# Kernel tuning notes

Hardware: AMD Instinct MI355X
Metric: run time of the kernel (lower is better)

Reference implementation:

```python
import jax, jax.numpy as jnp
import numpy as np

B, S, D_IN, E, H = 2, 2048, 1024, 1024, 16  # batch, seq, input_size, embedding_size, heads


def setup_inputs() -> dict:
    key = jax.random.key(0)
    k1, k2, k3 = jax.random.split(key, 3)
    x = jax.random.normal(k1, (B, S, D_IN), dtype=jnp.float32)
    # fused QKV projection weight stored as [in, 3E] (torch Linear weight transposed)
    W0 = jax.random.normal(k2, (D_IN, 3 * E), dtype=jnp.float32) * (1.0 / np.sqrt(D_IN))
    b0 = jax.random.normal(k3, (3 * E,), dtype=jnp.float32) * 0.02
    return {"x": x, "W0": W0, "b0": b0}


def reference(x, W0, b0):
    b, s, _ = x.shape
    y = x @ W0 + b0                              # [B,S,3E]
    y = y.reshape(b, s, H, -1).transpose(0, 2, 1, 3)  # [B,H,S,3*head_dim]
    q, k, v = jnp.split(y, 3, axis=-1)           # each [B,H,S,head_dim]
    scale = 1.0 / jnp.sqrt(jnp.asarray(D_IN, dtype=x.dtype))  # NB: sqrt(input_size), as in source
    scores = jnp.einsum("bhqd,bhkd->bhqk", q, k) * scale
    # causal mask: -inf above diagonal
    causal = jnp.triu(jnp.full((s, s), -jnp.inf, dtype=scores.dtype), k=1)
    scores = scores + causal
    attn = jax.nn.softmax(scores, axis=-1)       # [B,H,S,S]
    o = jnp.einsum("bhqk,bhkd->bhqd", attn, v)   # [B,H,S,head_dim]
    # faithful to source: reshape directly from (B,H,S,d) to (B,S,H*d) WITHOUT permuting back
    return o.reshape(b, s, -1)
```

## Files before the change

kernel.cpp:

```cpp
#include <hip/hip_runtime.h>
#include <stdint.h>

typedef __attribute__((ext_vector_type(4))) float f32x4;
typedef __attribute__((ext_vector_type(16))) float f32x16;
typedef __attribute__((ext_vector_type(8))) short bf16x8;
typedef __attribute__((ext_vector_type(4))) short bf16x4;

#define MFMA16(a, b, c) __builtin_amdgcn_mfma_f32_16x16x32_bf16((a), (b), (c), 0, 0, 0)
#define MFMA32(a, b, c) __builtin_amdgcn_mfma_f32_32x32x16_bf16((a), (b), (c), 0, 0, 0)

__device__ __forceinline__ short f2bf(float f) {
    union { float f; uint32_t u; } v; v.f = f;
    uint32_t r = (v.u + 0x7fffu + ((v.u >> 16) & 1u)) >> 16;
    return (short)(uint16_t)r;
}
__device__ __forceinline__ float bf2f(short s) {
    union { uint32_t u; float f; } v; v.u = ((uint32_t)(uint16_t)s) << 16;
    return v.f;
}
__device__ __forceinline__ float fast_exp2(float x) {
    float r; asm("v_exp_f32 %0, %1" : "=v"(r) : "v"(x)); return r;
}

__device__ __forceinline__ void async_ld16(const short* g, short* l) {
    __builtin_amdgcn_global_load_lds(
        (const __attribute__((address_space(1))) uint32_t*)g,
        (__attribute__((address_space(3))) uint32_t*)l, 16, 0, 0);
}

#define MK_BFRAG(C, O, OUT) do {                                                   \
    uint32_t a_, b_, c_, d_;                                                       \
    asm("v_cvt_pk_bf16_f32 %0, %1, %2" : "=v"(a_) : "v"((C)[(O)+0]), "v"((C)[(O)+1])); \
    asm("v_cvt_pk_bf16_f32 %0, %1, %2" : "=v"(c_) : "v"((C)[(O)+2]), "v"((C)[(O)+3])); \
    asm("v_cvt_pk_bf16_f32 %0, %1, %2" : "=v"(b_) : "v"((C)[(O)+4]), "v"((C)[(O)+5])); \
    asm("v_cvt_pk_bf16_f32 %0, %1, %2" : "=v"(d_) : "v"((C)[(O)+6]), "v"((C)[(O)+7])); \
    asm("v_permlane32_swap_b32 %0, %1" : "+v"(a_), "+v"(b_));                      \
    asm("v_permlane32_swap_b32 %0, %1" : "+v"(c_), "+v"(d_));                      \
    union { uint32_t u[4]; bf16x8 v; } pb_;                                        \
    pb_.u[0] = a_; pb_.u[1] = c_; pb_.u[2] = b_; pb_.u[3] = d_;                    \
    OUT = pb_.v;                                                                   \
} while (0)

__global__ __launch_bounds__(256)
void convert_x(const float* __restrict__ X, short* __restrict__ Xb) {
    const int i8 = (blockIdx.x * 256 + threadIdx.x) << 3;
    f32x4 a = *(const f32x4*)(X + i8);
    f32x4 b = *(const f32x4*)(X + i8 + 4);
    bf16x8 o;
#pragma unroll
    for (int j = 0; j < 4; ++j) { o[j] = f2bf(a[j]); o[4 + j] = f2bf(b[j]); }
    *(bf16x8*)(Xb + i8) = o;
}

__global__ __launch_bounds__(256)
void convert_wt(const float* __restrict__ W, short* __restrict__ Wt) {
    __shared__ short T[64][72];
    const int t = threadIdx.x;
    const int n0 = blockIdx.x * 64, k0 = blockIdx.y * 64;
#pragma unroll
    for (int i = 0; i < 4; ++i) {
        const int r = i * 16 + (t >> 4);
        const int c = (t & 15) << 2;
        f32x4 v = *(const f32x4*)(W + (size_t)(k0 + r) * 3072 + n0 + c);
#pragma unroll
        for (int j = 0; j < 4; ++j) T[c + j][r] = f2bf(v[j]);
    }
    __syncthreads();
#pragma unroll
    for (int i = 0; i < 2; ++i) {
        const int r = i * 32 + (t >> 3);
        const int c = (t & 7) << 3;
        *(bf16x8*)(Wt + (size_t)(n0 + r) * 1024 + k0 + c) = *(const bf16x8*)&T[r][c];
    }
}

__global__ __launch_bounds__(256, 3)
void gemm_pack(const short* __restrict__ Xb, const short* __restrict__ Wt,
               const float* __restrict__ bias, short* __restrict__ Qp,
               short* __restrict__ Kp, short* __restrict__ Vp) {
    __shared__ short Asm[3][128 * 32];
    __shared__ short Bsm[3][128 * 32];

    const int tid  = threadIdx.x;
    const int lane = tid & 63;
    const int l15  = lane & 15;
    const int lq   = lane >> 4;
    const int wave = tid >> 6;
    const int wr = wave >> 1, wc = wave & 1;

    const int bid = blockIdx.x;
    const int swz = (bid & 7) * 96 + (bid >> 3);
    const int m0 = (swz / 24) * 128, n0 = (swz % 24) * 128;

    const int srow = tid >> 2;
    const int scolsw = (((tid & 3) ^ (srow & 3)) << 3);

    f32x4 acc[4][4];
#pragma unroll
    for (int m = 0; m < 4; ++m)
#pragma unroll
        for (int n = 0; n < 4; ++n) acc[m][n] = (f32x4)(0.0f);

    auto stage = [&](int k0, int bb) {
#pragma unroll
        for (int i = 0; i < 2; ++i)
            async_ld16(Xb + (size_t)(m0 + i * 64 + srow) * 1024 + k0 + scolsw,
                       &Asm[bb][(i * 256 + wave * 64) * 8]);
#pragma unroll
        for (int i = 0; i < 2; ++i)
            async_ld16(Wt + (size_t)(n0 + i * 64 + srow) * 1024 + k0 + scolsw,
                       &Bsm[bb][(i * 256 + wave * 64) * 8]);
    };

    const int gsw = ((lq ^ (l15 & 3)) << 3);

    auto compute = [&](int bb) {
        bf16x8 af[4], bfv[4];
#pragma unroll
        for (int m = 0; m < 4; ++m)
            af[m] = *(const bf16x8*)&Asm[bb][(wr * 64 + m * 16 + l15) * 32 + gsw];
#pragma unroll
        for (int n = 0; n < 4; ++n)
            bfv[n] = *(const bf16x8*)&Bsm[bb][(wc * 64 + n * 16 + l15) * 32 + gsw];
#pragma unroll
        for (int m = 0; m < 4; ++m)
#pragma unroll
            for (int n = 0; n < 4; ++n) acc[m][n] = MFMA16(af[m], bfv[n], acc[m][n]);
    };

#define WAITV(N) do {                                           \
        asm volatile("s_waitcnt vmcnt(" #N ")" ::: "memory");   \
        __builtin_amdgcn_sched_barrier(0);                      \
        __builtin_amdgcn_s_barrier();                           \
        __builtin_amdgcn_sched_barrier(0);                      \
    } while (0)

    stage(0, 0);
    stage(32, 1);
#pragma unroll 1
    for (int kt = 0; kt < 30; ++kt) {
        WAITV(4);
        compute(kt % 3);
        stage((kt + 2) * 32, (kt + 2) % 3);
    }
    WAITV(4);
    compute(0);
    WAITV(0);
    compute(1);
#undef WAITV

    const float SCALE2 = 0.03125f * 1.44269504f;
    float bv[4];
#pragma unroll
    for (int n = 0; n < 4; ++n) bv[n] = bias[n0 + wc * 64 + n * 16 + l15];

    const size_t bbase = (size_t)(m0 >> 11) * 2097152;
    const int tokb = (m0 & 2047) + wr * 64;

#pragma unroll
    for (int n = 0; n < 4; ++n) {
        const int col = n0 + wc * 64 + n * 16 + l15;
        const int h   = col / 192;
        const int seg = (col >> 6) % 3;
        const int d   = col & 63;
        const size_t hb = bbase + (size_t)h * 131072;
        if (seg == 0) {
            const int cp = ((d >> 4) << 9) + (((d >> 3) & 1) << 8) + (d & 7);
#pragma unroll
            for (int m = 0; m < 4; ++m)
#pragma unroll
                for (int r = 0; r < 4; ++r) {
                    const int tok = tokb + m * 16 + (lq << 2) + r;
                    Qp[hb + ((size_t)(tok >> 5) << 11) + ((tok & 31) << 3) + cp] =
                        f2bf((acc[m][n][r] + bv[n]) * SCALE2);
                }
        } else if (seg == 1) {
            const int cp = ((d >> 4) << 10) + (((d >> 3) & 1) << 8) + (d & 7);
#pragma unroll
            for (int m = 0; m < 4; ++m)
#pragma unroll
                for (int r = 0; r < 4; ++r) {
                    const int tok = tokb + m * 16 + (lq << 2) + r;
                    Kp[hb + ((size_t)(tok >> 6) << 12) + (((tok >> 5) & 1) << 9)
                       + ((tok & 31) << 3) + cp] = f2bf(acc[m][n][r] + bv[n]);
                }
        } else {
            const int cp = ((d >> 5) << 11) + ((d & 31) << 3);
#pragma unroll
            for (int m = 0; m < 4; ++m)
#pragma unroll
                for (int r = 0; r < 4; ++r) {
                    const int tok = tokb + m * 16 + (lq << 2) + r;
                    Vp[hb + ((size_t)(tok >> 6) << 12) + (((tok >> 4) & 3) << 9)
                       + (((tok >> 3) & 1) << 8) + (tok & 7) + cp] =
                        f2bf(acc[m][n][r] + bv[n]);
                }
        }
    }
}

__global__ __launch_bounds__(64, 2)
void attn_part(const short* __restrict__ Qp, const short* __restrict__ Kp,
               const short* __restrict__ Vp, short* __restrict__ Po,
               float* __restrict__ Pm) {
    const int tid = threadIdx.x;
    const int l31 = tid & 31;
    const int hi  = tid >> 5;

    const int id  = blockIdx.x;
    const int xcd = id & 7;
    const int idx = id >> 3;
    const int bh  = xcd * 4 + idx / 96;
    const int u   = idx % 96;

    int qt, t0, t1;
    if (u < 32)      { qt = u + 32; t0 = 0;  t1 = 16; }
    else if (u < 64) { qt = 95 - u; t0 = 16; t1 = (qt >> 1) + 1; }
    else             { qt = u - 64; t0 = 0;  t1 = (qt >> 1) + 1; }
    const bool hasDiag = (u >= 32);
    const int q0 = qt * 32;

    const size_t hb = (size_t)bh * 131072;

    bf16x8 qf[4];
    {
        const short* qp = Qp + hb + qt * 2048 + tid * 8;
#pragma unroll
        for (int dg = 0; dg < 4; ++dg) qf[dg] = *(const bf16x8*)(qp + dg * 512);
    }

    f32x16 o0 = (f32x16)(0.f), o1 = (f32x16)(0.f);
    float m_run = -1e30f, l_run = 0.f;
    const int qg = q0 + l31;

    bf16x8 kA[8], kB[8], va[8];

    auto loadK = [&](bf16x8 (&kr)[8], int t) {
        const short* p = Kp + hb + (size_t)t * 4096 + tid * 8;
#pragma unroll
        for (int f = 0; f < 8; ++f)
            kr[f] = *(const bf16x8*)(p + (f >> 1) * 1024 + (f & 1) * 512);
    };
    auto loadV = [&](int t) {
        const short* p = Vp + hb + (size_t)t * 4096 + tid * 8;
#pragma unroll
        for (int f = 0; f < 8; ++f) va[f] = *(const bf16x8*)(p + f * 512);
    };
    auto qk = [&](bf16x8 (&kr)[8], f32x16& c0, f32x16& c1) {
#pragma unroll
        for (int dg = 0; dg < 4; ++dg) {
            c0 = MFMA32(kr[2 * dg],     qf[dg], c0);
            c1 = MFMA32(kr[2 * dg + 1], qf[dg], c1);
        }
    };

    auto smpv = [&](f32x16& c0, f32x16& c1, int kv0, bool DIAG) {
        if (DIAG) {
#pragma unroll
            for (int r = 0; r < 16; ++r) {
                const int kvr = kv0 + (r & 3) + 8 * (r >> 2) + 4 * hi;
                if (kvr > qg)      c0[r] = -1e30f;
                if (kvr + 32 > qg) c1[r] = -1e30f;
            }
        }

        float mr[8];
#pragma unroll
        for (int r = 0; r < 8; ++r)
            mr[r] = fmaxf(fmaxf(c0[r], c0[8 + r]), fmaxf(c1[r], c1[8 + r]));
        float mx = fmaxf(fmaxf(fmaxf(mr[0], mr[1]), fmaxf(mr[2], mr[3])),
                         fmaxf(fmaxf(mr[4], mr[5]), fmaxf(mr[6], mr[7])));
        mx = fmaxf(mx, __shfl_xor(mx, 32, 64));

        if (!__all(mx <= m_run + 8.f)) {
            const float mnew = fmaxf(m_run, mx);
            const float corr = fast_exp2(m_run - mnew);
            l_run *= corr;
            o0 = o0 * corr;
            o1 = o1 * corr;
            m_run = mnew;
        }

        float ps0 = 0.f, ps1 = 0.f, ps2 = 0.f, ps3 = 0.f;
#pragma unroll
        for (int r = 0; r < 4; ++r) {
            c0[r]      = fast_exp2(c0[r]      - m_run); ps0 += c0[r];
            c0[4 + r]  = fast_exp2(c0[4 + r]  - m_run); ps1 += c0[4 + r];
            c0[8 + r]  = fast_exp2(c0[8 + r]  - m_run); ps2 += c0[8 + r];
            c0[12 + r] = fast_exp2(c0[12 + r] - m_run); ps3 += c0[12 + r];
        }
#pragma unroll
        for (int r = 0; r < 4; ++r) {
            c1[r]      = fast_exp2(c1[r]      - m_run); ps0 += c1[r];
            c1[4 + r]  = fast_exp2(c1[4 + r]  - m_run); ps1 += c1[4 + r];
            c1[8 + r]  = fast_exp2(c1[8 + r]  - m_run); ps2 += c1[8 + r];
            c1[12 + r] = fast_exp2(c1[12 + r] - m_run); ps3 += c1[12 + r];
        }
        l_run += (ps0 + ps1) + (ps2 + ps3);

        bf16x8 bf00, bf01, bf10, bf11;
        MK_BFRAG(c0, 0, bf00);
        MK_BFRAG(c0, 8, bf01);
        MK_BFRAG(c1, 0, bf10);
        MK_BFRAG(c1, 8, bf11);

        o0 = MFMA32(va[0], bf00, o0);
        o0 = MFMA32(va[1], bf01, o0);
        o0 = MFMA32(va[2], bf10, o0);
        o0 = MFMA32(va[3], bf11, o0);
        o1 = MFMA32(va[4], bf00, o1);
        o1 = MFMA32(va[5], bf01, o1);
        o1 = MFMA32(va[6], bf10, o1);
        o1 = MFMA32(va[7], bf11, o1);
    };

    int t = t0;
    loadK(kA, t0);
#pragma unroll 1
    for (; t + 2 < t1; t += 2) {
        f32x16 c0 = (f32x16)(0.f), c1 = (f32x16)(0.f);
        qk(kA, c0, c1);
        loadK(kB, t + 1);
        loadV(t);
        smpv(c0, c1, t * 64, false);
        f32x16 d0 = (f32x16)(0.f), d1 = (f32x16)(0.f);
        qk(kB, d0, d1);
        loadK(kA, t + 2);
        loadV(t + 1);
        smpv(d0, d1, (t + 1) * 64, false);
    }
    if (t + 1 < t1) {
        f32x16 c0 = (f32x16)(0.f), c1 = (f32x16)(0.f);
        qk(kA, c0, c1);
        loadK(kB, t + 1);
        loadV(t);
        smpv(c0, c1, t * 64, false);
        f32x16 d0 = (f32x16)(0.f), d1 = (f32x16)(0.f);
        qk(kB, d0, d1);
        loadV(t + 1);
        smpv(d0, d1, (t + 1) * 64, hasDiag);
    } else {
        f32x16 c0 = (f32x16)(0.f), c1 = (f32x16)(0.f);
        qk(kA, c0, c1);
        loadV(t);
        smpv(c0, c1, t * 64, hasDiag);
    }

    const float l_tot = l_run + __shfl_xor(l_run, 32, 64);
    const float inv = 1.f / l_tot;
    const int prow = (bh * 96 + u) * 32 + l31;
#pragma unroll
    for (int g = 0; g < 4; ++g) {
        bf16x4 w4;
#pragma unroll
        for (int j = 0; j < 4; ++j) w4[j] = f2bf(o0[g * 4 + j] * inv);
        *(bf16x4*)&Po[(size_t)prow * 64 + 8 * g + 4 * hi] = w4;
#pragma unroll
        for (int j = 0; j < 4; ++j) w4[j] = f2bf(o1[g * 4 + j] * inv);
        *(bf16x4*)&Po[(size_t)prow * 64 + 32 + 8 * g + 4 * hi] = w4;
    }
    if (hi == 0) Pm[prow] = m_run + __log2f(l_tot);
}

__global__ __launch_bounds__(256)
void attn_combine(const short* __restrict__ Po, const float* __restrict__ Pm,
                  float* __restrict__ Out) {
    const int idx = blockIdx.x * 256 + threadIdx.x;
    const int d4 = (idx & 15) << 2;
    const int rg = idx >> 4;
    const int q  = rg & 2047;
    const int bh = rg >> 11;
    const int qt32 = q >> 5, r = q & 31;

    f32x4 ov;
    if (qt32 < 32) {
        const int p0 = (bh * 96 + 64 + qt32) * 32 + r;
        bf16x4 a = *(const bf16x4*)&Po[(size_t)p0 * 64 + d4];
#pragma unroll
        for (int j = 0; j < 4; ++j) ov[j] = bf2f(a[j]);
    } else {
        const int p0 = (bh * 96 + (qt32 - 32)) * 32 + r;
        const int p1 = (bh * 96 + (95 - qt32)) * 32 + r;
        bf16x4 a = *(const bf16x4*)&Po[(size_t)p0 * 64 + d4];
        bf16x4 c = *(const bf16x4*)&Po[(size_t)p1 * 64 + d4];
        const float m0 = Pm[p0], m1 = Pm[p1];
        const float M = fmaxf(m0, m1);
        const float w0 = exp2f(m0 - M), w1 = exp2f(m1 - M);
        const float inv = 1.f / (w0 + w1);
#pragma unroll
        for (int j = 0; j < 4; ++j) ov[j] = (w0 * bf2f(a[j]) + w1 * bf2f(c[j])) * inv;
    }
    *(f32x4*)&Out[(size_t)rg * 64 + d4] = ov;
}

extern "C" void kernel_launch(void* const* d_in, const int* in_sizes, int n_in,
                              void* d_out, int out_size, void* d_ws, size_t ws_size,
                              hipStream_t stream) {
    const float* x  = (const float*)d_in[0];
    const float* W0 = (const float*)d_in[1];
    const float* b0 = (const float*)d_in[2];
    float* out = (float*)d_out;
    char* ws = (char*)d_ws;

    const size_t SEG_B = (size_t)32 * 131072 * 2;
    const size_t QKV_B = 3 * SEG_B;
    const size_t XBF_B = (size_t)4096 * 1024 * 2;
    const size_t PO_B  = (size_t)32 * 96 * 32 * 64 * 2;

    short* qp = (short*)ws;
    short* kp = (short*)(ws + SEG_B);
    short* vp = (short*)(ws + 2 * SEG_B);
    short* xb = (short*)(ws + QKV_B);
    short* wt = (short*)(ws + QKV_B + XBF_B);
    short* po = (short*)(ws + QKV_B);
    float* pm = (float*)(ws + QKV_B + PO_B);

    convert_x<<<dim3(2048), dim3(256), 0, stream>>>(x, xb);
    convert_wt<<<dim3(48, 16), dim3(256), 0, stream>>>(W0, wt);
    gemm_pack<<<dim3(768), dim3(256), 0, stream>>>(xb, wt, b0, qp, kp, vp);
    attn_part<<<dim3(3072), dim3(64), 0, stream>>>(qp, kp, vp, po, pm);
    attn_combine<<<dim3(4096), dim3(256), 0, stream>>>(po, pm, out);
}
```

Measured before the change: 94.53 us.

## Fuse conversion kernels and pack four heads per attention block

Merges the x and weight bf16 conversion kernels into a single launch, with blocks beyond 2048 handling the weight transpose. It also changes attn_part from 64-thread blocks to 256-thread blocks, where each wave handles a different head for the same query-tile schedule, cutting the grid from 3072 to 768 blocks. The aim is less launch overhead and fewer, larger workgroups. The cost is that the four waves in a block run independent work with no shared data, so a block holds its CU slot until its slowest wave finishes. Occupancy now depends on the (256,2) launch bound rather than the old (64,2).

```diff
diff --git a/kernel.cpp b/kernel.cpp
--- a/kernel.cpp
+++ b/kernel.cpp
@@ -42,21 +42,23 @@
 } while (0)
 
 __global__ __launch_bounds__(256)
-void convert_x(const float* __restrict__ X, short* __restrict__ Xb) {
-    const int i8 = (blockIdx.x * 256 + threadIdx.x) << 3;
-    f32x4 a = *(const f32x4*)(X + i8);
-    f32x4 b = *(const f32x4*)(X + i8 + 4);
-    bf16x8 o;
-#pragma unroll
-    for (int j = 0; j < 4; ++j) { o[j] = f2bf(a[j]); o[4 + j] = f2bf(b[j]); }
-    *(bf16x8*)(Xb + i8) = o;
-}
-
-__global__ __launch_bounds__(256)
-void convert_wt(const float* __restrict__ W, short* __restrict__ Wt) {
+void convert_fused(const float* __restrict__ X, short* __restrict__ Xb,
+                   const float* __restrict__ W, short* __restrict__ Wt) {
     __shared__ short T[64][72];
     const int t = threadIdx.x;
-    const int n0 = blockIdx.x * 64, k0 = blockIdx.y * 64;
+    const int id = blockIdx.x;
+    if (id < 2048) {
+        const int i8 = (id * 256 + t) << 3;
+        f32x4 a = *(const f32x4*)(X + i8);
+        f32x4 b = *(const f32x4*)(X + i8 + 4);
+        bf16x8 o;
+#pragma unroll
+        for (int j = 0; j < 4; ++j) { o[j] = f2bf(a[j]); o[4 + j] = f2bf(b[j]); }
+        *(bf16x8*)(Xb + i8) = o;
+        return;
+    }
+    const int wid = id - 2048;
+    const int n0 = (wid % 48) * 64, k0 = (wid / 48) * 64;
 #pragma unroll
     for (int i = 0; i < 4; ++i) {
         const int r = i * 16 + (t >> 4);
@@ -199,19 +201,20 @@
     }
 }
 
-__global__ __launch_bounds__(64, 2)
+__global__ __launch_bounds__(256, 2)
 void attn_part(const short* __restrict__ Qp, const short* __restrict__ Kp,
                const short* __restrict__ Vp, short* __restrict__ Po,
                float* __restrict__ Pm) {
-    const int tid = threadIdx.x;
-    const int l31 = tid & 31;
-    const int hi  = tid >> 5;
+    const int tid  = threadIdx.x;
+    const int lane = tid & 63;
+    const int l31  = lane & 31;
+    const int hi   = (lane >> 5) & 1;
+    const int w    = tid >> 6;
 
     const int id  = blockIdx.x;
     const int xcd = id & 7;
-    const int idx = id >> 3;
-    const int bh  = xcd * 4 + idx / 96;
-    const int u   = idx % 96;
+    const int u   = id >> 3;
+    const int bh  = xcd * 4 + w;
 
     int qt, t0, t1;
     if (u < 32)      { qt = u + 32; t0 = 0;  t1 = 16; }
@@ -224,7 +227,7 @@
 
     bf16x8 qf[4];
     {
-        const short* qp = Qp + hb + qt * 2048 + tid * 8;
+        const short* qp = Qp + hb + qt * 2048 + lane * 8;
 #pragma unroll
         for (int dg = 0; dg < 4; ++dg) qf[dg] = *(const bf16x8*)(qp + dg * 512);
     }
@@ -236,13 +239,13 @@
     bf16x8 kA[8], kB[8], va[8];
 
     auto loadK = [&](bf16x8 (&kr)[8], int t) {
-        const short* p = Kp + hb + (size_t)t * 4096 + tid * 8;
+        const short* p = Kp + hb + (size_t)t * 4096 + lane * 8;
 #pragma unroll
         for (int f = 0; f < 8; ++f)
             kr[f] = *(const bf16x8*)(p + (f >> 1) * 1024 + (f & 1) * 512);
     };
     auto loadV = [&](int t) {
-        const short* p = Vp + hb + (size_t)t * 4096 + tid * 8;
+        const short* p = Vp + hb + (size_t)t * 4096 + lane * 8;
 #pragma unroll
         for (int f = 0; f < 8; ++f) va[f] = *(const bf16x8*)(p + f * 512);
     };
@@ -415,9 +418,8 @@
     short* po = (short*)(ws + QKV_B);
     float* pm = (float*)(ws + QKV_B + PO_B);
 
-    convert_x<<<dim3(2048), dim3(256), 0, stream>>>(x, xb);
-    convert_wt<<<dim3(48, 16), dim3(256), 0, stream>>>(W0, wt);
+    convert_fused<<<dim3(2816), dim3(256), 0, stream>>>(x, xb, W0, wt);
     gemm_pack<<<dim3(768), dim3(256), 0, stream>>>(xb, wt, b0, qp, kp, vp);
-    attn_part<<<dim3(3072), dim3(64), 0, stream>>>(qp, kp, vp, po, pm);
+    attn_part<<<dim3(768), dim3(256), 0, stream>>>(qp, kp, vp, po, pm);
     attn_combine<<<dim3(4096), dim3(256), 0, stream>>>(po, pm, out);
 }
```

New measurement: 94.04 us. Within noise of the previous version (-0.5%).

## Fuse conversion kernels, reorder attention work items, raise attn occupancy

Applied to the files above, without the earlier changes.

Merges the x and weight conversion kernels into one launch, removing one kernel launch and its tail. Reorders the attention work-item mapping so heads are interleaved within each XCD and diagonal tiles are grouped by cost, with the combine kernel's index math updated to match. Raises attn_part's waves-per-EU hint from 2 to 4, which may force register spills in exchange for more resident waves.

```diff
diff --git a/kernel.cpp b/kernel.cpp
--- a/kernel.cpp
+++ b/kernel.cpp
@@ -42,21 +42,23 @@
 } while (0)
 
 __global__ __launch_bounds__(256)
-void convert_x(const float* __restrict__ X, short* __restrict__ Xb) {
-    const int i8 = (blockIdx.x * 256 + threadIdx.x) << 3;
-    f32x4 a = *(const f32x4*)(X + i8);
-    f32x4 b = *(const f32x4*)(X + i8 + 4);
-    bf16x8 o;
-#pragma unroll
-    for (int j = 0; j < 4; ++j) { o[j] = f2bf(a[j]); o[4 + j] = f2bf(b[j]); }
-    *(bf16x8*)(Xb + i8) = o;
-}
-
-__global__ __launch_bounds__(256)
-void convert_wt(const float* __restrict__ W, short* __restrict__ Wt) {
+void convert_fused(const float* __restrict__ X, short* __restrict__ Xb,
+                   const float* __restrict__ W, short* __restrict__ Wt) {
     __shared__ short T[64][72];
     const int t = threadIdx.x;
-    const int n0 = blockIdx.x * 64, k0 = blockIdx.y * 64;
+    const int id = blockIdx.x;
+    if (id < 2048) {
+        const int i8 = (id * 256 + t) << 3;
+        f32x4 a = *(const f32x4*)(X + i8);
+        f32x4 b = *(const f32x4*)(X + i8 + 4);
+        bf16x8 o;
+#pragma unroll
+        for (int j = 0; j < 4; ++j) { o[j] = f2bf(a[j]); o[4 + j] = f2bf(b[j]); }
+        *(bf16x8*)(Xb + i8) = o;
+        return;
+    }
+    const int wid = id - 2048;
+    const int n0 = (wid % 48) * 64, k0 = (wid / 48) * 64;
 #pragma unroll
     for (int i = 0; i < 4; ++i) {
         const int r = i * 16 + (t >> 4);
@@ -199,7 +201,7 @@
     }
 }
 
-__global__ __launch_bounds__(64, 2)
+__global__ __launch_bounds__(64, 4)
 void attn_part(const short* __restrict__ Qp, const short* __restrict__ Kp,
                const short* __restrict__ Vp, short* __restrict__ Po,
                float* __restrict__ Pm) {
@@ -210,14 +212,20 @@
     const int id  = blockIdx.x;
     const int xcd = id & 7;
     const int idx = id >> 3;
-    const int bh  = xcd * 4 + idx / 96;
-    const int u   = idx % 96;
+    const int u   = idx >> 2;
+    const int bh  = xcd * 4 + (idx & 3);
 
     int qt, t0, t1;
-    if (u < 32)      { qt = u + 32; t0 = 0;  t1 = 16; }
-    else if (u < 64) { qt = 95 - u; t0 = 16; t1 = (qt >> 1) + 1; }
-    else             { qt = u - 64; t0 = 0;  t1 = (qt >> 1) + 1; }
-    const bool hasDiag = (u >= 32);
+    bool hasDiag;
+    if (u < 32) {
+        qt = u + 32; t0 = 0; t1 = 16; hasDiag = false;
+    } else {
+        const int s = 16 - ((u - 32) >> 2);
+        const int j = (u - 32) & 3;
+        if (j < 2) { qt = 2 * s - 2 + j;       t0 = 0;  t1 = s; }
+        else       { qt = 2 * s + 30 + (j - 2); t0 = 16; t1 = s + 16; }
+        hasDiag = true;
+    }
     const int q0 = qt * 32;
 
     const size_t hb = (size_t)bh * 131072;
@@ -357,7 +365,7 @@
         *(bf16x4*)&Po[(size_t)prow * 64 + 8 * g + 4 * hi] = w4;
 #pragma unroll
         for (int j = 0; j < 4; ++j) w4[j] = f2bf(o1[g * 4 + j] * inv);
-        *(bf16x4*)&Po[(size_t)prow * 64 + 32 + 8 * g + 4 * hi] = w4;
+        *(bf16x4*)&Po[(size_t)prow * 64 + 32 + 4 * hi + 8 * g] = w4;
     }
     if (hi == 0) Pm[prow] = m_run + __log2f(l_tot);
 }
@@ -370,17 +378,22 @@
     const int rg = idx >> 4;
     const int q  = rg & 2047;
     const int bh = rg >> 11;
-    const int qt32 = q >> 5, r = q & 31;
+    const int qt = q >> 5, r = q & 31;
 
     f32x4 ov;
-    if (qt32 < 32) {
-        const int p0 = (bh * 96 + 64 + qt32) * 32 + r;
+    if (qt < 32) {
+        const int s = (qt >> 1) + 1;
+        const int u = 32 + (16 - s) * 4 + (qt & 1);
+        const int p0 = (bh * 96 + u) * 32 + r;
         bf16x4 a = *(const bf16x4*)&Po[(size_t)p0 * 64 + d4];
 #pragma unroll
         for (int j = 0; j < 4; ++j) ov[j] = bf2f(a[j]);
     } else {
-        const int p0 = (bh * 96 + (qt32 - 32)) * 32 + r;
-        const int p1 = (bh * 96 + (95 - qt32)) * 32 + r;
+        const int u0 = qt - 32;
+        const int s  = (qt >> 1) - 15;
+        const int u1 = 32 + (16 - s) * 4 + 2 + (qt & 1);
+        const int p0 = (bh * 96 + u0) * 32 + r;
+        const int p1 = (bh * 96 + u1) * 32 + r;
         bf16x4 a = *(const bf16x4*)&Po[(size_t)p0 * 64 + d4];
         bf16x4 c = *(const bf16x4*)&Po[(size_t)p1 * 64 + d4];
         const float m0 = Pm[p0], m1 = Pm[p1];
@@ -415,8 +428,7 @@
     short* po = (short*)(ws + QKV_B);
     float* pm = (float*)(ws + QKV_B + PO_B);
 
-    convert_x<<<dim3(2048), dim3(256), 0, stream>>>(x, xb);
-    convert_wt<<<dim3(48, 16), dim3(256), 0, stream>>>(W0, wt);
+    convert_fused<<<dim3(2816), dim3(256), 0, stream>>>(x, xb, W0, wt);
     gemm_pack<<<dim3(768), dim3(256), 0, stream>>>(xb, wt, b0, qp, kp, vp);
     attn_part<<<dim3(3072), dim3(64), 0, stream>>>(qp, kp, vp, po, pm);
     attn_combine<<<dim3(4096), dim3(256), 0, stream>>>(po, pm, out);
```

Result: slower. 180.7 us (+91.1%).
